# Kernel optimization log

Hardware: AMD Instinct MI355X
Metric: run time of the kernel (lower is better)

## Reference

```python
import jax, jax.numpy as jnp
import numpy as np

N = 100000
E = 1250000
D = 64
POS_DIM = 3


def _linear_params(key, fan_in, fan_out, bias=True):
    k1, k2 = jax.random.split(key)
    bound = 1.0 / np.sqrt(fan_in)
    W = jax.random.uniform(k1, (fan_in, fan_out), minval=-bound, maxval=bound, dtype=jnp.float32)
    if bias:
        b = jax.random.uniform(k2, (fan_out,), minval=-bound, maxval=bound, dtype=jnp.float32)
        return W, b
    return W


def setup_inputs() -> dict:
    key = jax.random.key(0)
    ks = jax.random.split(key, 10)
    x = jax.random.normal(ks[0], (N, D), dtype=jnp.float32)
    pos = jax.random.normal(ks[1], (N, POS_DIM), dtype=jnp.float32)
    edge_index = jax.random.randint(ks[2], (2, E), 0, N, dtype=jnp.int64)
    W_in, b_in = _linear_params(ks[3], D, D)
    W_lin = _linear_params(ks[4], D, D, bias=False)
    W_src = _linear_params(ks[5], D, D, bias=False)
    W_dst = _linear_params(ks[6], D, D, bias=False)
    W_pos, b_pos = _linear_params(ks[7], POS_DIM, D)
    W_out, b_out = _linear_params(ks[8], D, D)
    return {"x": x, "pos": pos, "edge_index": edge_index,
            "W_in": W_in, "b_in": b_in, "W_lin": W_lin, "W_src": W_src,
            "W_dst": W_dst, "W_pos": W_pos, "b_pos": b_pos,
            "W_out": W_out, "b_out": b_out}


def reference(x, pos, edge_index, W_in, b_in, W_lin, W_src, W_dst, W_pos, b_pos, W_out, b_out):
    n = x.shape[0]
    src, dst = edge_index[0], edge_index[1]  # j, i (PyG source_to_target)
    # lin_in + relu
    h = jax.nn.relu(x @ W_in + b_in)  # [N, D]
    # PointTransformerConv projections
    x_lin = h @ W_lin      # value projection, gathered at src (x_j)
    a_src = h @ W_src      # alpha_j side
    a_dst = h @ W_dst      # alpha_i side
    # per-edge positional MLP on pos_i - pos_j
    delta = (pos[dst] - pos[src]) @ W_pos + b_pos  # [E, D]
    # per-edge attention logits, per channel
    alpha = a_dst[dst] - a_src[src] + delta  # [E, D]
    # segment softmax over destination node groups (PyG softmax, eps=1e-16)
    seg_max = jax.ops.segment_max(alpha, dst, num_segments=n)
    alpha = jnp.exp(alpha - seg_max[dst])
    seg_sum = jax.ops.segment_sum(alpha, dst, num_segments=n)
    alpha = alpha / (seg_sum[dst] + 1e-16)
    # weighted messages, scatter-add aggregate
    msg = alpha * (x_lin[src] + delta)  # [E, D]
    out = jax.ops.segment_sum(msg, dst, num_segments=n)  # [N, D]
    # lin_out + relu
    return jax.nn.relu(out @ W_out + b_out)
```

## Files before the change

### kernel.cpp

```cpp
#include <hip/hip_runtime.h>

#define NN 100000
#define NE 1250000
#define NWIN 782
#define GA 256
#define CHUNK ((NE + GA - 1) / GA)
#define CAP16 16
#define OVFCAP 131072
#define WEDCAP 40

typedef __attribute__((ext_vector_type(4))) float f32x4;
typedef __attribute__((ext_vector_type(8))) short s16x8;

__device__ __forceinline__ short bfb(float f) {
    union { float f; unsigned u; } c; c.f = f;
    unsigned u = c.u + 0x7fffu + ((c.u >> 16) & 1u);
    return (short)(u >> 16);
}
__device__ __forceinline__ void splitbf(float v, short& hi, short& lo) {
    hi = bfb(v);
    union { unsigned u; float f; } c; c.u = ((unsigned)(unsigned short)hi) << 16;
    lo = bfb(v - c.f);
}
__device__ __forceinline__ float lo2f(unsigned u) {
    union { unsigned u; float f; } c; c.u = u << 16; return c.f;
}
__device__ __forceinline__ float hi2f(unsigned u) {
    union { unsigned u; float f; } c; c.u = u & 0xffff0000u; return c.f;
}

__global__ __launch_bounds__(256) void k_prep(
    const float* __restrict__ Wi, const float* __restrict__ Wl,
    const float* __restrict__ Ws, const float* __restrict__ Wo,
    short* __restrict__ P, int* __restrict__ ovf_cnt)
{
    const int t = blockIdx.x * 256 + threadIdx.x;
    if (t == 0) *ovf_cnt = 0;
    if (t >= 2048) return;
    const int mat = t >> 9, rem = t & 511;
    const int lane = rem & 63, cfg = rem >> 6;
    const int kh = cfg >> 2, nt = cfg & 3;
    const int m = lane & 15, q = lane >> 4;
    const float* W = mat == 0 ? Wi : mat == 1 ? Wl : mat == 2 ? Ws : Wo;
    s16x8 v;
    #pragma unroll
    for (int i = 0; i < 8; ++i)
        v[i] = bfb(W[(kh * 32 + q * 8 + i) * 64 + nt * 16 + m]);
    *(s16x8*)&P[(size_t)t * 8] = v;
}

__global__ __launch_bounds__(256) void k_node_in(
    const float* __restrict__ x, const short* __restrict__ P,
    const float* __restrict__ b_in,
    const float* __restrict__ pos, const float* __restrict__ W_pos,
    unsigned* __restrict__ AXb)
{
    __shared__ float hT[4][16 * 68];
    const int lane = threadIdx.x & 63;
    const int wid  = threadIdx.x >> 6;
    const int m = lane & 15, q = lane >> 4;

    s16x8 Wf[3][2][4];
    #pragma unroll
    for (int mat = 0; mat < 3; ++mat)
        #pragma unroll
        for (int kh = 0; kh < 2; ++kh)
            #pragma unroll
            for (int nt = 0; nt < 4; ++nt)
                Wf[mat][kh][nt] = *(const s16x8*)&P[((size_t)mat * 512 + (kh * 4 + nt) * 64 + lane) * 8];
    float bin[4], wpv0[4], wpv1[4], wpv2[4];
    #pragma unroll
    for (int nt = 0; nt < 4; ++nt) {
        bin[nt]  = b_in[nt * 16 + m];
        wpv0[nt] = W_pos[nt * 16 + m];
        wpv1[nt] = W_pos[64 + nt * 16 + m];
        wpv2[nt] = W_pos[128 + nt * 16 + m];
    }

    const int wave = blockIdx.x * 4 + wid, nw = gridDim.x * 4;
    for (int chunk = wave; chunk < NN / 16; chunk += nw) {
        const int r0 = chunk * 16;
        const float* xr = x + (size_t)(r0 + m) * 64;
        float xv[16];
        *(float4*)&xv[0]  = *(const float4*)(xr + q * 8);
        *(float4*)&xv[4]  = *(const float4*)(xr + q * 8 + 4);
        *(float4*)&xv[8]  = *(const float4*)(xr + 32 + q * 8);
        *(float4*)&xv[12] = *(const float4*)(xr + 32 + q * 8 + 4);
        s16x8 ahi0, alo0, ahi1, alo1;
        #pragma unroll
        for (int i = 0; i < 8; ++i) {
            short h, l;
            splitbf(xv[i], h, l);     ahi0[i] = h; alo0[i] = l;
            splitbf(xv[8 + i], h, l); ahi1[i] = h; alo1[i] = l;
        }
        #pragma unroll
        for (int nt = 0; nt < 4; ++nt) {
            f32x4 acc = {0.f, 0.f, 0.f, 0.f};
            acc = __builtin_amdgcn_mfma_f32_16x16x32_bf16(alo0, Wf[0][0][nt], acc, 0, 0, 0);
            acc = __builtin_amdgcn_mfma_f32_16x16x32_bf16(alo1, Wf[0][1][nt], acc, 0, 0, 0);
            acc = __builtin_amdgcn_mfma_f32_16x16x32_bf16(ahi0, Wf[0][0][nt], acc, 0, 0, 0);
            acc = __builtin_amdgcn_mfma_f32_16x16x32_bf16(ahi1, Wf[0][1][nt], acc, 0, 0, 0);
            #pragma unroll
            for (int r = 0; r < 4; ++r) {
                float hv = acc[r] + bin[nt];
                hT[wid][(q * 4 + r) * 68 + nt * 16 + m] = hv > 0.f ? hv : 0.f;
            }
        }
        float hv[16];
        *(float4*)&hv[0]  = *(const float4*)&hT[wid][m * 68 + q * 8];
        *(float4*)&hv[4]  = *(const float4*)&hT[wid][m * 68 + q * 8 + 4];
        *(float4*)&hv[8]  = *(const float4*)&hT[wid][m * 68 + 32 + q * 8];
        *(float4*)&hv[12] = *(const float4*)&hT[wid][m * 68 + 32 + q * 8 + 4];
        s16x8 hhi0, hlo0, hhi1, hlo1;
        #pragma unroll
        for (int i = 0; i < 8; ++i) {
            short h, l;
            splitbf(hv[i], h, l);     hhi0[i] = h; hlo0[i] = l;
            splitbf(hv[8 + i], h, l); hhi1[i] = h; hlo1[i] = l;
        }
        float px[4], py[4], pz[4];
        #pragma unroll
        for (int r = 0; r < 4; ++r) {
            const float* pp = pos + (size_t)(r0 + q * 4 + r) * 3;
            px[r] = pp[0]; py[r] = pp[1]; pz[r] = pp[2];
        }
        #pragma unroll
        for (int nt = 0; nt < 4; ++nt) {
            f32x4 aS = {0.f, 0.f, 0.f, 0.f}, aL = {0.f, 0.f, 0.f, 0.f};
            aS = __builtin_amdgcn_mfma_f32_16x16x32_bf16(hlo0, Wf[2][0][nt], aS, 0, 0, 0);
            aS = __builtin_amdgcn_mfma_f32_16x16x32_bf16(hlo1, Wf[2][1][nt], aS, 0, 0, 0);
            aS = __builtin_amdgcn_mfma_f32_16x16x32_bf16(hhi0, Wf[2][0][nt], aS, 0, 0, 0);
            aS = __builtin_amdgcn_mfma_f32_16x16x32_bf16(hhi1, Wf[2][1][nt], aS, 0, 0, 0);
            aL = __builtin_amdgcn_mfma_f32_16x16x32_bf16(hlo0, Wf[1][0][nt], aL, 0, 0, 0);
            aL = __builtin_amdgcn_mfma_f32_16x16x32_bf16(hlo1, Wf[1][1][nt], aL, 0, 0, 0);
            aL = __builtin_amdgcn_mfma_f32_16x16x32_bf16(hhi0, Wf[1][0][nt], aL, 0, 0, 0);
            aL = __builtin_amdgcn_mfma_f32_16x16x32_bf16(hhi1, Wf[1][1][nt], aL, 0, 0, 0);
            #pragma unroll
            for (int r = 0; r < 4; ++r) {
                const float sp = fmaf(px[r], wpv0[nt], fmaf(py[r], wpv1[nt], pz[r] * wpv2[nt]));
                const unsigned p = (unsigned)(unsigned short)bfb(aS[r] + sp)
                                 | ((unsigned)(unsigned short)bfb(aL[r] - sp) << 16);
                AXb[(size_t)(r0 + q * 4 + r) * 64 + nt * 16 + m] = p;
            }
        }
    }
}

__global__ __launch_bounds__(256) void k_passA(
    const int* __restrict__ ei, unsigned* __restrict__ stage, int* __restrict__ gcnt,
    int2* __restrict__ ovf, int* __restrict__ ovf_cnt)
{
    __shared__ int lcnt[NWIN];
    const int g = blockIdx.x;
    for (int i = threadIdx.x; i < NWIN; i += 256) lcnt[i] = 0;
    __syncthreads();
    unsigned* myStage = stage + (size_t)g * NWIN * CAP16;
    const int e0 = g * CHUNK;
    const int e1 = (e0 + CHUNK < NE) ? e0 + CHUNK : NE;
    for (int e = e0 + threadIdx.x; e < e1; e += 256) {
        const int s = ei[e], d = ei[NE + e];
        const int b = d >> 7;
        const int c = atomicAdd(&lcnt[b], 1);
        if (c < CAP16) {
            myStage[b * CAP16 + c] = (unsigned)s | ((unsigned)(d & 127) << 17);
        } else {
            const int o = atomicAdd(ovf_cnt, 1);
            if (o < OVFCAP) ovf[o] = make_int2(s, d);
        }
    }
    __syncthreads();
    for (int i = threadIdx.x; i < NWIN; i += 256)
        gcnt[i * GA + g] = lcnt[i] < CAP16 ? lcnt[i] : CAP16;
}

__global__ __launch_bounds__(256) void k_passB(
    const unsigned* __restrict__ stage, const int* __restrict__ gcnt,
    const int2* __restrict__ ovf, const int* __restrict__ ovf_cnt,
    int* __restrict__ slots, int* __restrict__ deg)
{
    __shared__ int slotsL[128 * WEDCAP];
    __shared__ int cntL[128];
    const int b = blockIdx.x;
    const int t = threadIdx.x;
    if (t < 128) cntL[t] = 0;
    __syncthreads();
    const int n = min(gcnt[b * GA + t], CAP16);
    const unsigned* cell = stage + (size_t)t * NWIN * CAP16 + b * CAP16;
    uint4 q0 = *(const uint4*)cell;
    uint4 q1 = *(const uint4*)(cell + 4);
    uint4 q2 = *(const uint4*)(cell + 8);
    uint4 q3 = *(const uint4*)(cell + 12);
    const unsigned eb[16] = {q0.x, q0.y, q0.z, q0.w, q1.x, q1.y, q1.z, q1.w,
                             q2.x, q2.y, q2.z, q2.w, q3.x, q3.y, q3.z, q3.w};
    #pragma unroll
    for (int i = 0; i < CAP16; ++i)
        if (i < n) {
            const int d7 = (int)(eb[i] >> 17);
            const int c = atomicAdd(&cntL[d7], 1);
            if (c < WEDCAP) slotsL[d7 * WEDCAP + c] = (int)(eb[i] & 0x1ffff);
        }
    const int no = min(*ovf_cnt, OVFCAP);
    for (int i = t; i < no; i += 256) {
        const int2 sd = ovf[i];
        if ((sd.y >> 7) == b) {
            const int d7 = sd.y & 127;
            const int c = atomicAdd(&cntL[d7], 1);
            if (c < WEDCAP) slotsL[d7 * WEDCAP + c] = sd.x;
        }
    }
    __syncthreads();
    int4* dstq = (int4*)(slots + (size_t)b * 128 * WEDCAP);
    const int4* srcq = (const int4*)slotsL;
    #pragma unroll
    for (int i = 0; i < 5; ++i) dstq[i * 256 + t] = srcq[i * 256 + t];
    if (t < 128) {
        const int d = (b << 7) + t;
        if (d < NN) deg[d] = cntL[t] < WEDCAP ? cntL[t] : WEDCAP;
    }
}

__global__ __launch_bounds__(256) void k_agg(
    const int* __restrict__ deg_arr, const int* __restrict__ slots,
    const float* __restrict__ pos,
    const float* __restrict__ W_pos, const float* __restrict__ b_pos,
    const unsigned* __restrict__ AXb, float* __restrict__ V)
{
    const int lane = threadIdx.x & 63;
    const int d = __builtin_amdgcn_readfirstlane((int)((blockIdx.x * 256 + threadIdx.x) >> 6));
    if (d >= NN) return;
    const float pd0 = pos[d * 3 + 0], pd1 = pos[d * 3 + 1], pd2 = pos[d * 3 + 2];
    const float dlb = fmaf(pd0, W_pos[lane],
                      fmaf(pd1, W_pos[64 + lane],
                      fmaf(pd2, W_pos[128 + lane], b_pos[lane])));

    int deg = deg_arr[d]; deg = deg < WEDCAP ? deg : WEDCAP;
    const int* srow = slots + (size_t)d * WEDCAP;

    float Sa = 0.f, Ua = 0.f;
    if (deg > 0) {
        int cs[4], ns[4];
        unsigned cax[4], nax[4];
        {
            const int4 qd = *(const int4*)srow;
            cs[0] = qd.x;
            cs[1] = (1 < deg) ? qd.y : qd.x;
            cs[2] = (2 < deg) ? qd.z : qd.x;
            cs[3] = (3 < deg) ? qd.w : qd.x;
            #pragma unroll
            for (int k = 0; k < 4; ++k)
                cax[k] = AXb[(size_t)cs[k] * 64 + lane];
        }
        for (int j = 0; j < deg; j += 8) {
            if (j + 4 < deg) {
                const int4 qd = *(const int4*)(srow + j + 4);
                ns[0] = qd.x;
                ns[1] = (j + 5 < deg) ? qd.y : qd.x;
                ns[2] = (j + 6 < deg) ? qd.z : qd.x;
                ns[3] = (j + 7 < deg) ? qd.w : qd.x;
                #pragma unroll
                for (int k = 0; k < 4; ++k)
                    nax[k] = AXb[(size_t)ns[k] * 64 + lane];
            }
            #pragma unroll
            for (int k = 0; k < 4; ++k) {
                float wv = __expf(dlb - lo2f(cax[k]));
                if (j + k >= deg) wv = 0.f;
                Sa += wv;
                Ua = fmaf(wv, hi2f(cax[k]) + dlb, Ua);
            }
            if (j + 8 < deg) {
                const int4 qd = *(const int4*)(srow + j + 8);
                cs[0] = qd.x;
                cs[1] = (j + 9  < deg) ? qd.y : qd.x;
                cs[2] = (j + 10 < deg) ? qd.z : qd.x;
                cs[3] = (j + 11 < deg) ? qd.w : qd.x;
                #pragma unroll
                for (int k = 0; k < 4; ++k)
                    cax[k] = AXb[(size_t)cs[k] * 64 + lane];
            }
            if (j + 4 < deg) {
                #pragma unroll
                for (int k = 0; k < 4; ++k) {
                    float wv = __expf(dlb - lo2f(nax[k]));
                    if (j + 4 + k >= deg) wv = 0.f;
                    Sa += wv;
                    Ua = fmaf(wv, hi2f(nax[k]) + dlb, Ua);
                }
            }
        }
    }
    V[(size_t)d * 64 + lane] = Ua / (Sa + 1e-16f);
}

__global__ __launch_bounds__(256) void k_node_out(
    const float* __restrict__ V, const short* __restrict__ P,
    const float* __restrict__ b_out, float* __restrict__ out)
{
    const int lane = threadIdx.x & 63;
    const int wid  = threadIdx.x >> 6;
    const int m = lane & 15, q = lane >> 4;

    s16x8 Wf[2][4];
    #pragma unroll
    for (int kh = 0; kh < 2; ++kh)
        #pragma unroll
        for (int nt = 0; nt < 4; ++nt)
            Wf[kh][nt] = *(const s16x8*)&P[((size_t)3 * 512 + (kh * 4 + nt) * 64 + lane) * 8];
    float bo[4];
    #pragma unroll
    for (int nt = 0; nt < 4; ++nt) bo[nt] = b_out[nt * 16 + m];

    const int wave = blockIdx.x * 4 + wid, nw = gridDim.x * 4;
    for (int chunk = wave; chunk < NN / 16; chunk += nw) {
        const int r0 = chunk * 16;
        const float* vr = V + (size_t)(r0 + m) * 64;
        float vv[16];
        *(float4*)&vv[0]  = *(const float4*)(vr + q * 8);
        *(float4*)&vv[4]  = *(const float4*)(vr + q * 8 + 4);
        *(float4*)&vv[8]  = *(const float4*)(vr + 32 + q * 8);
        *(float4*)&vv[12] = *(const float4*)(vr + 32 + q * 8 + 4);
        s16x8 ahi0, alo0, ahi1, alo1;
        #pragma unroll
        for (int i = 0; i < 8; ++i) {
            short h, l;
            splitbf(vv[i], h, l);     ahi0[i] = h; alo0[i] = l;
            splitbf(vv[8 + i], h, l); ahi1[i] = h; alo1[i] = l;
        }
        #pragma unroll
        for (int nt = 0; nt < 4; ++nt) {
            f32x4 acc = {0.f, 0.f, 0.f, 0.f};
            acc = __builtin_amdgcn_mfma_f32_16x16x32_bf16(alo0, Wf[0][nt], acc, 0, 0, 0);
            acc = __builtin_amdgcn_mfma_f32_16x16x32_bf16(alo1, Wf[1][nt], acc, 0, 0, 0);
            acc = __builtin_amdgcn_mfma_f32_16x16x32_bf16(ahi0, Wf[0][nt], acc, 0, 0, 0);
            acc = __builtin_amdgcn_mfma_f32_16x16x32_bf16(ahi1, Wf[1][nt], acc, 0, 0, 0);
            #pragma unroll
            for (int r = 0; r < 4; ++r) {
                float o = acc[r] + bo[nt];
                out[(size_t)(r0 + q * 4 + r) * 64 + nt * 16 + m] = o > 0.f ? o : 0.f;
            }
        }
    }
}

extern "C" void kernel_launch(void* const* d_in, const int* in_sizes, int n_in,
                              void* d_out, int out_size, void* d_ws, size_t ws_size,
                              hipStream_t stream) {
    const float* x     = (const float*)d_in[0];
    const float* pos   = (const float*)d_in[1];
    const int*   ei    = (const int*)d_in[2];
    const float* W_in  = (const float*)d_in[3];
    const float* b_in  = (const float*)d_in[4];
    const float* W_lin = (const float*)d_in[5];
    const float* W_src = (const float*)d_in[6];
    const float* W_pos = (const float*)d_in[8];
    const float* b_pos = (const float*)d_in[9];
    const float* W_out = (const float*)d_in[10];
    const float* b_out = (const float*)d_in[11];

    unsigned* AXb   = (unsigned*)d_ws;
    unsigned* stage = AXb + (size_t)NN * 64;
    int*      gcnt  = (int*)(stage + (size_t)GA * NWIN * CAP16);
    int*      slots = gcnt + (size_t)NWIN * GA;
    int*      deg   = slots + (size_t)NWIN * 128 * WEDCAP;
    float*    V     = (float*)(deg + NN);
    int2*     ovf   = (int2*)(V + (size_t)NN * 64);
    int*      ovfc  = (int*)(ovf + OVFCAP);
    short*    P     = (short*)(ovfc + 64);

    k_prep    <<<8,    256, 0, stream>>>(W_in, W_lin, W_src, W_out, P, ovfc);
    k_node_in <<<512,  256, 0, stream>>>(x, P, b_in, pos, W_pos, AXb);
    k_passA   <<<GA,   256, 0, stream>>>(ei, stage, gcnt, ovf, ovfc);
    k_passB   <<<NWIN, 256, 0, stream>>>(stage, gcnt, ovf, ovfc, slots, deg);
    k_agg     <<<(NN + 3) / 4, 256, 0, stream>>>(deg, slots, pos, W_pos, b_pos, AXb, V);
    k_node_out<<<512,  256, 0, stream>>>(V, P, b_out, (float*)d_out);
}
```

Before: 188.7 us.

## Fuse edge aggregation with output projection via shared-memory tile

Merges the per-node aggregation kernel and the output linear+ReLU kernel into one. Each block aggregates 16 destination nodes (4 per wave), stores the results in a padded shared-memory tile, then one wave runs the MFMA output projection directly from shared memory. This removes the V intermediate's global write and read-back plus one kernel launch. The cost is that three of the four waves sit idle during the MFMA phase, and per-wave parallelism over nodes drops, which may hurt latency hiding in the gather loop.

```diff
diff --git a/kernel.cpp b/kernel.cpp
--- a/kernel.cpp
+++ b/kernel.cpp
@@ -219,106 +219,105 @@
     }
 }
 
-__global__ __launch_bounds__(256) void k_agg(
+__global__ __launch_bounds__(256, 8) void k_aggout(
     const int* __restrict__ deg_arr, const int* __restrict__ slots,
     const float* __restrict__ pos,
     const float* __restrict__ W_pos, const float* __restrict__ b_pos,
-    const unsigned* __restrict__ AXb, float* __restrict__ V)
-{
+    const unsigned* __restrict__ AXb,
+    const short* __restrict__ P, const float* __restrict__ b_out,
+    float* __restrict__ out)
+{
+    __shared__ float Vt[16 * 68];
     const int lane = threadIdx.x & 63;
-    const int d = __builtin_amdgcn_readfirstlane((int)((blockIdx.x * 256 + threadIdx.x) >> 6));
-    if (d >= NN) return;
-    const float pd0 = pos[d * 3 + 0], pd1 = pos[d * 3 + 1], pd2 = pos[d * 3 + 2];
-    const float dlb = fmaf(pd0, W_pos[lane],
-                      fmaf(pd1, W_pos[64 + lane],
-                      fmaf(pd2, W_pos[128 + lane], b_pos[lane])));
-
-    int deg = deg_arr[d]; deg = deg < WEDCAP ? deg : WEDCAP;
-    const int* srow = slots + (size_t)d * WEDCAP;
-
-    float Sa = 0.f, Ua = 0.f;
-    if (deg > 0) {
-        int cs[4], ns[4];
-        unsigned cax[4], nax[4];
-        {
-            const int4 qd = *(const int4*)srow;
-            cs[0] = qd.x;
-            cs[1] = (1 < deg) ? qd.y : qd.x;
-            cs[2] = (2 < deg) ? qd.z : qd.x;
-            cs[3] = (3 < deg) ? qd.w : qd.x;
-            #pragma unroll
-            for (int k = 0; k < 4; ++k)
-                cax[k] = AXb[(size_t)cs[k] * 64 + lane];
-        }
-        for (int j = 0; j < deg; j += 8) {
-            if (j + 4 < deg) {
-                const int4 qd = *(const int4*)(srow + j + 4);
-                ns[0] = qd.x;
-                ns[1] = (j + 5 < deg) ? qd.y : qd.x;
-                ns[2] = (j + 6 < deg) ? qd.z : qd.x;
-                ns[3] = (j + 7 < deg) ? qd.w : qd.x;
-                #pragma unroll
-                for (int k = 0; k < 4; ++k)
-                    nax[k] = AXb[(size_t)ns[k] * 64 + lane];
-            }
-            #pragma unroll
-            for (int k = 0; k < 4; ++k) {
-                float wv = __expf(dlb - lo2f(cax[k]));
-                if (j + k >= deg) wv = 0.f;
-                Sa += wv;
-                Ua = fmaf(wv, hi2f(cax[k]) + dlb, Ua);
-            }
-            if (j + 8 < deg) {
-                const int4 qd = *(const int4*)(srow + j + 8);
+    const int wid  = threadIdx.x >> 6;
+    const int m = lane & 15, q = lane >> 4;
+    const int dbase = blockIdx.x * 16;
+
+    const float wpl0 = W_pos[lane], wpl1 = W_pos[64 + lane], wpl2 = W_pos[128 + lane];
+    const float bpl  = b_pos[lane];
+
+    #pragma unroll 1
+    for (int i = 0; i < 4; ++i) {
+        const int d = dbase + wid * 4 + i;
+        const float pd0 = pos[d * 3 + 0], pd1 = pos[d * 3 + 1], pd2 = pos[d * 3 + 2];
+        const float dlb = fmaf(pd0, wpl0, fmaf(pd1, wpl1, fmaf(pd2, wpl2, bpl)));
+
+        int deg = deg_arr[d]; deg = deg < WEDCAP ? deg : WEDCAP;
+        const int* srow = slots + (size_t)d * WEDCAP;
+
+        float Sa = 0.f, Ua = 0.f;
+        if (deg > 0) {
+            int cs[4], ns[4];
+            unsigned cax[4], nax[4];
+            {
+                const int4 qd = *(const int4*)srow;
                 cs[0] = qd.x;
-                cs[1] = (j + 9  < deg) ? qd.y : qd.x;
-                cs[2] = (j + 10 < deg) ? qd.z : qd.x;
-                cs[3] = (j + 11 < deg) ? qd.w : qd.x;
+                cs[1] = (1 < deg) ? qd.y : qd.x;
+                cs[2] = (2 < deg) ? qd.z : qd.x;
+                cs[3] = (3 < deg) ? qd.w : qd.x;
                 #pragma unroll
                 for (int k = 0; k < 4; ++k)
                     cax[k] = AXb[(size_t)cs[k] * 64 + lane];
             }
-            if (j + 4 < deg) {
+            for (int j = 0; j < deg; j += 8) {
+                if (j + 4 < deg) {
+                    const int4 qd = *(const int4*)(srow + j + 4);
+                    ns[0] = qd.x;
+                    ns[1] = (j + 5 < deg) ? qd.y : qd.x;
+                    ns[2] = (j + 6 < deg) ? qd.z : qd.x;
+                    ns[3] = (j + 7 < deg) ? qd.w : qd.x;
+                    #pragma unroll
+                    for (int k = 0; k < 4; ++k)
+                        nax[k] = AXb[(size_t)ns[k] * 64 + lane];
+                }
                 #pragma unroll
                 for (int k = 0; k < 4; ++k) {
-                    float wv = __expf(dlb - lo2f(nax[k]));
-                    if (j + 4 + k >= deg) wv = 0.f;
+                    float wv = __expf(dlb - lo2f(cax[k]));
+                    if (j + k >= deg) wv = 0.f;
                     Sa += wv;
-                    Ua = fmaf(wv, hi2f(nax[k]) + dlb, Ua);
+                    Ua = fmaf(wv, hi2f(cax[k]) + dlb, Ua);
                 }
-            }
-        }
-    }
-    V[(size_t)d * 64 + lane] = Ua / (Sa + 1e-16f);
-}
-
-__global__ __launch_bounds__(256) void k_node_out(
-    const float* __restrict__ V, const short* __restrict__ P,
-    const float* __restrict__ b_out, float* __restrict__ out)
-{
-    const int lane = threadIdx.x & 63;
-    const int wid  = threadIdx.x >> 6;
-    const int m = lane & 15, q = lane >> 4;
-
-    s16x8 Wf[2][4];
-    #pragma unroll
-    for (int kh = 0; kh < 2; ++kh)
-        #pragma unroll
-        for (int nt = 0; nt < 4; ++nt)
-            Wf[kh][nt] = *(const s16x8*)&P[((size_t)3 * 512 + (kh * 4 + nt) * 64 + lane) * 8];
-    float bo[4];
-    #pragma unroll
-    for (int nt = 0; nt < 4; ++nt) bo[nt] = b_out[nt * 16 + m];
-
-    const int wave = blockIdx.x * 4 + wid, nw = gridDim.x * 4;
-    for (int chunk = wave; chunk < NN / 16; chunk += nw) {
-        const int r0 = chunk * 16;
-        const float* vr = V + (size_t)(r0 + m) * 64;
+                if (j + 8 < deg) {
+                    const int4 qd = *(const int4*)(srow + j + 8);
+                    cs[0] = qd.x;
+                    cs[1] = (j + 9  < deg) ? qd.y : qd.x;
+                    cs[2] = (j + 10 < deg) ? qd.z : qd.x;
+                    cs[3] = (j + 11 < deg) ? qd.w : qd.x;
+                    #pragma unroll
+                    for (int k = 0; k < 4; ++k)
+                        cax[k] = AXb[(size_t)cs[k] * 64 + lane];
+                }
+                if (j + 4 < deg) {
+                    #pragma unroll
+                    for (int k = 0; k < 4; ++k) {
+                        float wv = __expf(dlb - lo2f(nax[k]));
+                        if (j + 4 + k >= deg) wv = 0.f;
+                        Sa += wv;
+                        Ua = fmaf(wv, hi2f(nax[k]) + dlb, Ua);
+                    }
+                }
+            }
+        }
+        Vt[(wid * 4 + i) * 68 + lane] = Ua / (Sa + 1e-16f);
+    }
+    __syncthreads();
+
+    if (wid == 0) {
+        s16x8 Wf[2][4];
+        #pragma unroll
+        for (int kh = 0; kh < 2; ++kh)
+            #pragma unroll
+            for (int nt = 0; nt < 4; ++nt)
+                Wf[kh][nt] = *(const s16x8*)&P[((size_t)3 * 512 + (kh * 4 + nt) * 64 + lane) * 8];
+        float bo[4];
+        #pragma unroll
+        for (int nt = 0; nt < 4; ++nt) bo[nt] = b_out[nt * 16 + m];
+
         float vv[16];
-        *(float4*)&vv[0]  = *(const float4*)(vr + q * 8);
-        *(float4*)&vv[4]  = *(const float4*)(vr + q * 8 + 4);
-        *(float4*)&vv[8]  = *(const float4*)(vr + 32 + q * 8);
-        *(float4*)&vv[12] = *(const float4*)(vr + 32 + q * 8 + 4);
+        *(float4*)&vv[0]  = *(const float4*)&Vt[m * 68 + q * 8];
+        *(float4*)&vv[4]  = *(const float4*)&Vt[m * 68 + q * 8 + 4];
+        *(float4*)&vv[8]  = *(const float4*)&Vt[m * 68 + 32 + q * 8];
+        *(float4*)&vv[12] = *(const float4*)&Vt[m * 68 + 32 + q * 8 + 4];
         s16x8 ahi0, alo0, ahi1, alo1;
         #pragma unroll
         for (int i = 0; i < 8; ++i) {
@@ -335,8 +334,8 @@
             acc = __builtin_amdgcn_mfma_f32_16x16x32_bf16(ahi1, Wf[1][nt], acc, 0, 0, 0);
             #pragma unroll
             for (int r = 0; r < 4; ++r) {
-                float o = acc[r] + bo[nt];
-                out[(size_t)(r0 + q * 4 + r) * 64 + nt * 16 + m] = o > 0.f ? o : 0.f;
+                const float o = acc[r] + bo[nt];
+                out[(size_t)(dbase + q * 4 + r) * 64 + nt * 16 + m] = o > 0.f ? o : 0.f;
             }
         }
     }
@@ -362,15 +361,13 @@
     int*      gcnt  = (int*)(stage + (size_t)GA * NWIN * CAP16);
     int*      slots = gcnt + (size_t)NWIN * GA;
     int*      deg   = slots + (size_t)NWIN * 128 * WEDCAP;
-    float*    V     = (float*)(deg + NN);
-    int2*     ovf   = (int2*)(V + (size_t)NN * 64);
+    int2*     ovf   = (int2*)(deg + NN);
     int*      ovfc  = (int*)(ovf + OVFCAP);
     short*    P     = (short*)(ovfc + 64);
 
-    k_prep    <<<8,    256, 0, stream>>>(W_in, W_lin, W_src, W_out, P, ovfc);
-    k_node_in <<<512,  256, 0, stream>>>(x, P, b_in, pos, W_pos, AXb);
-    k_passA   <<<GA,   256, 0, stream>>>(ei, stage, gcnt, ovf, ovfc);
-    k_passB   <<<NWIN, 256, 0, stream>>>(stage, gcnt, ovf, ovfc, slots, deg);
-    k_agg     <<<(NN + 3) / 4, 256, 0, stream>>>(deg, slots, pos, W_pos, b_pos, AXb, V);
-    k_node_out<<<512,  256, 0, stream>>>(V, P, b_out, (float*)d_out);
-}
+    k_prep   <<<8,     256, 0, stream>>>(W_in, W_lin, W_src, W_out, P, ovfc);
+    k_node_in<<<512,   256, 0, stream>>>(x, P, b_in, pos, W_pos, AXb);
+    k_passA  <<<GA,    256, 0, stream>>>(ei, stage, gcnt, ovf, ovfc);
+    k_passB  <<<NWIN,  256, 0, stream>>>(stage, gcnt, ovf, ovfc, slots, deg);
+    k_aggout <<<NN/16, 256, 0, stream>>>(deg, slots, pos, W_pos, b_pos, AXb, P, b_out, (float*)d_out);
+}
```

After: 193.3 us. 1.02x slower.
